# Kernel tuning notes

Measured on AMD Instinct MI355X. Metric: run time of the kernel, lower is better.

## Reference

```python
import jax, jax.numpy as jnp
import numpy as np
import math

B, I, O, D, H = 32, 1152, 10, 16, 10
SUB = 0.8
S = math.ceil(SUB * I)  # 922 subset size


def _safe_l2norm(x, axis, keepdims=False):
    # L2 norm with zero-safe gradient (forward-identical to jnp.linalg.norm)
    s = jnp.sum(x * x, axis=axis, keepdims=keepdims)
    return jnp.where(s == 0, 0.0, jnp.sqrt(jnp.where(s == 0, 1.0, s)))


def setup_inputs() -> dict:
    key = jax.random.key(0)
    k1, k2 = jax.random.split(key)
    u_predict = jax.random.normal(k1, (B, I, O, D), dtype=jnp.float32)
    # emulate torch.rand(...).topk(S, dim=1).indices: top-S distinct indices along input_caps
    noise = jax.random.uniform(k2, (B, I, O, H))
    sample_idx = jnp.argsort(-noise, axis=1)[:, :S].astype(jnp.int64)  # [B,S,O,H]
    return {"u_predict": u_predict, "sample_idx": sample_idx}


def reference(u_predict, sample_idx):
    b, i, o, d = u_predict.shape
    h = sample_idx.shape[-1]
    # scatter 0/1 hypothesis mask r: [B,I,O,H]
    bi = jnp.arange(b)[:, None, None, None]
    oi = jnp.arange(o)[None, None, :, None]
    hi = jnp.arange(h)[None, None, None, :]
    r = jnp.zeros((b, i, o, h), u_predict.dtype).at[bi, sample_idx, oi, hi].set(1.0)

    # Vr = V_exp * r; since r is 0/1, ||Vr||_D = r * ||V||_D
    Vnorm = _safe_l2norm(u_predict, axis=3)            # [B,I,O]
    Vr_norm = Vnorm[..., None] * r                     # [B,I,O,H]
    # Mu = sum_i(Vr_norm * Vr) / sum_i Vr_norm  (Vr_norm*Vr = r*||V||*V since r^2=r)
    num = jnp.einsum('bioh,biod->bodh', Vr_norm, u_predict)   # [B,O,D,H]
    Mu = num / jnp.sum(Vr_norm, axis=1)[:, :, None, :]        # [B,O,D,H]

    # losses = sum_i ||V_exp - Mu||_D  -> [B,O,H]
    diff = u_predict[..., None] - Mu[:, None]          # [B,I,O,D,H]
    losses = jnp.sum(_safe_l2norm(diff, axis=3), axis=1)
    min_idx = jnp.argmin(losses, axis=2)               # [B,O]

    # pick best hypothesis's mask per (batch, output_caps)
    final_r = jnp.take_along_axis(r, min_idx[:, None, :, None], axis=3)  # [B,I,O,1]

    # capsule weighted average
    u = u_predict * final_r
    un = _safe_l2norm(u, axis=3, keepdims=True)        # [B,I,O,1]
    v = jnp.sum(u * un, axis=1) / jnp.sum(un, axis=1)  # [B,O,D]
    return v
```

## Files before the change

kernel.cpp:

```cpp
#include <hip/hip_runtime.h>
#include <math.h>


#define B_    32
#define I_    1152
#define O_    10
#define D_    16
#define H_    10
#define S_    922
#define MASKW 36
#define NT    384
#define NW    6
#define RPT   3
#define HH    11

template <int CTRL, int ROWM>
static __device__ __forceinline__ float dpp_f(float v) {
    return __int_as_float(__builtin_amdgcn_update_dpp(
        0, __float_as_int(v), CTRL, ROWM, 0xf, true));
}
static __device__ __forceinline__ float wave_sum_f32(float v) {
    v += dpp_f<0x111, 0xf>(v);
    v += dpp_f<0x112, 0xf>(v);
    v += dpp_f<0x114, 0xf>(v);
    v += dpp_f<0x118, 0xf>(v);
    v += dpp_f<0x142, 0xa>(v);
    v += dpp_f<0x143, 0xc>(v);
    return v;
}
template <int CTRL, int ROWM>
static __device__ __forceinline__ double dpp_d(double v) {
    long long x = __double_as_longlong(v);
    int lo = (int)(unsigned)(x & 0xffffffffLL);
    int hi = (int)(x >> 32);
    lo = __builtin_amdgcn_update_dpp(0, lo, CTRL, ROWM, 0xf, true);
    hi = __builtin_amdgcn_update_dpp(0, hi, CTRL, ROWM, 0xf, true);
    return __longlong_as_double((long long)(unsigned)lo | ((long long)hi << 32));
}
static __device__ __forceinline__ double wave_sum_f64(double v) {
    v += dpp_d<0x111, 0xf>(v);
    v += dpp_d<0x112, 0xf>(v);
    v += dpp_d<0x114, 0xf>(v);
    v += dpp_d<0x118, 0xf>(v);
    v += dpp_d<0x142, 0xa>(v);
    v += dpp_d<0x143, 0xc>(v);
    return v;
}

__global__ __launch_bounds__(NT, 3) void ransac_kernel(
    const float* __restrict__ up,
    const int*   __restrict__ sidx,
    float*       __restrict__ out)
{
    __shared__ unsigned                 mask[H_][MASKW];
    __shared__ __align__(16) float      hred[HH][NW][20];
    __shared__ float                    Mu_s[H_][D_];
    __shared__ double                   lpart[H_][NW];
    __shared__ double                   losses[H_];
    __shared__ int                      hstar;

    const int blk = blockIdx.x;
    const int xcd = blk & 7, g = blk >> 3;
    const int b   = xcd + 8 * (g / O_);
    const int o   = g - O_ * (g / O_);
    const int bo  = b * O_ + o;

    const int tid  = threadIdx.x;
    const int lane = tid & 63;
    const int wv   = tid >> 6;

    if (tid < H_ * MASKW) ((unsigned*)mask)[tid] = 0u;
    __syncthreads();

    const int* sb = sidx + (size_t)b * (S_ * O_ * H_) + o * H_;
    const bool p2 = tid < (S_ - 2 * NT);
    const int2* ps0 = (const int2*)(sb + (size_t)tid * (O_ * H_));
    const int2* ps1 = (const int2*)(sb + (size_t)(tid + NT) * (O_ * H_));
    int2 a0 = ps0[0], a1 = ps0[1], a2 = ps0[2], a3 = ps0[3], a4 = ps0[4];
    int2 b0 = ps1[0], b1 = ps1[1], b2 = ps1[2], b3 = ps1[3], b4 = ps1[4];
    int2 c0 = {0,0}, c1 = {0,0}, c2 = {0,0}, c3 = {0,0}, c4 = {0,0};
    if (p2) {
        const int2* ps2 = (const int2*)(sb + (size_t)(tid + 2 * NT) * (O_ * H_));
        c0 = ps2[0]; c1 = ps2[1]; c2 = ps2[2]; c3 = ps2[3]; c4 = ps2[4];
    }

    const float* ub = up + ((size_t)b * I_ * O_ + o) * D_;
    float4 R[RPT][4];
    #pragma unroll
    for (int r = 0; r < RPT; ++r) {
        const float4* p = (const float4*)(ub + (size_t)(tid + r * NT) * (O_ * D_));
        R[r][0] = p[0]; R[r][1] = p[1]; R[r][2] = p[2]; R[r][3] = p[3];
    }

    {
        int v0[H_] = {a0.x, a0.y, a1.x, a1.y, a2.x, a2.y, a3.x, a3.y, a4.x, a4.y};
        #pragma unroll
        for (int h = 0; h < H_; ++h)
            atomicOr(&mask[h][v0[h] >> 5], 1u << (v0[h] & 31));
        int v1[H_] = {b0.x, b0.y, b1.x, b1.y, b2.x, b2.y, b3.x, b3.y, b4.x, b4.y};
        #pragma unroll
        for (int h = 0; h < H_; ++h)
            atomicOr(&mask[h][v1[h] >> 5], 1u << (v1[h] & 31));
        if (p2) {
            int v2[H_] = {c0.x, c0.y, c1.x, c1.y, c2.x, c2.y, c3.x, c3.y, c4.x, c4.y};
            #pragma unroll
            for (int h = 0; h < H_; ++h)
                atomicOr(&mask[h][v2[h] >> 5], 1u << (v2[h] & 31));
        }
    }

    float vn[RPT], usq[RPT];
    #pragma unroll
    for (int r = 0; r < RPT; ++r) {
        float4 q0 = R[r][0], q1 = R[r][1], q2 = R[r][2], q3 = R[r][3];
        float s = q0.x*q0.x + q0.y*q0.y + q0.z*q0.z + q0.w*q0.w
                + q1.x*q1.x + q1.y*q1.y + q1.z*q1.z + q1.w*q1.w
                + q2.x*q2.x + q2.y*q2.y + q2.z*q2.z + q2.w*q2.w
                + q3.x*q3.x + q3.y*q3.y + q3.z*q3.z + q3.w*q3.w;
        vn[r] = sqrtf(s);
        float uq[D_] = {q0.x,q0.y,q0.z,q0.w, q1.x,q1.y,q1.z,q1.w,
                        q2.x,q2.y,q2.z,q2.w, q3.x,q3.y,q3.z,q3.w};
        float t = 0.f;
        #pragma unroll
        for (int d = 0; d < D_; ++d) t = fmaf(uq[d], uq[d], t);
        usq[r] = t;
    }
    __syncthreads();

    const int      w0   = tid >> 5;
    const unsigned bitm = 1u << (tid & 31);
    for (int h = 0; h < HH; ++h) {
        float na[17];
        #pragma unroll
        for (int d = 0; d < 17; ++d) na[d] = 0.f;
        #pragma unroll
        for (int r = 0; r < RPT; ++r) {
            float w = vn[r];
            if (h < H_) {
                unsigned mw = mask[h][w0 + 12 * r];
                w = (mw & bitm) ? 0.f : w;
            }
            float4 q0 = R[r][0], q1 = R[r][1], q2 = R[r][2], q3 = R[r][3];
            na[ 0] = fmaf(w, q0.x, na[ 0]); na[ 1] = fmaf(w, q0.y, na[ 1]);
            na[ 2] = fmaf(w, q0.z, na[ 2]); na[ 3] = fmaf(w, q0.w, na[ 3]);
            na[ 4] = fmaf(w, q1.x, na[ 4]); na[ 5] = fmaf(w, q1.y, na[ 5]);
            na[ 6] = fmaf(w, q1.z, na[ 6]); na[ 7] = fmaf(w, q1.w, na[ 7]);
            na[ 8] = fmaf(w, q2.x, na[ 8]); na[ 9] = fmaf(w, q2.y, na[ 9]);
            na[10] = fmaf(w, q2.z, na[10]); na[11] = fmaf(w, q2.w, na[11]);
            na[12] = fmaf(w, q3.x, na[12]); na[13] = fmaf(w, q3.y, na[13]);
            na[14] = fmaf(w, q3.z, na[14]); na[15] = fmaf(w, q3.w, na[15]);
            na[16] += w;
        }
        #pragma unroll
        for (int d = 0; d < 17; ++d) na[d] = wave_sum_f32(na[d]);
        if (lane == 63) {
            *(float4*)&hred[h][wv][ 0] = make_float4(na[ 0], na[ 1], na[ 2], na[ 3]);
            *(float4*)&hred[h][wv][ 4] = make_float4(na[ 4], na[ 5], na[ 6], na[ 7]);
            *(float4*)&hred[h][wv][ 8] = make_float4(na[ 8], na[ 9], na[10], na[11]);
            *(float4*)&hred[h][wv][12] = make_float4(na[12], na[13], na[14], na[15]);
            hred[h][wv][16] = na[16];
        }
    }
    __syncthreads();

    for (int h = wv; h < H_; h += NW) {
        if (lane < D_) {
            float naj = 0.f, totj = 0.f, na16 = 0.f, tot16 = 0.f;
            #pragma unroll
            for (int w = 0; w < NW; ++w) {
                naj   += hred[h ][w][lane];
                totj  += hred[10][w][lane];
                na16  += hred[h ][w][16];
                tot16 += hred[10][w][16];
            }
            float rd = 1.f / (tot16 - na16);
            Mu_s[h][lane] = (totj - naj) * rd;
        }
    }
    __syncthreads();

    for (int h = 0; h < H_; ++h) {
        float4 m0 = *(const float4*)&Mu_s[h][0];
        float4 m1 = *(const float4*)&Mu_s[h][4];
        float4 m2 = *(const float4*)&Mu_s[h][8];
        float4 m3 = *(const float4*)&Mu_s[h][12];
        float mv[D_] = {m0.x, m0.y, m0.z, m0.w, m1.x, m1.y, m1.z, m1.w,
                        m2.x, m2.y, m2.z, m2.w, m3.x, m3.y, m3.z, m3.w};
        float musq = 0.f;
        #pragma unroll
        for (int d = 0; d < D_; ++d) musq = fmaf(mv[d], mv[d], musq);
        double l = 0.0;
        #pragma unroll
        for (int r = 0; r < RPT; ++r) {
            float uq[D_] = {R[r][0].x, R[r][0].y, R[r][0].z, R[r][0].w,
                            R[r][1].x, R[r][1].y, R[r][1].z, R[r][1].w,
                            R[r][2].x, R[r][2].y, R[r][2].z, R[r][2].w,
                            R[r][3].x, R[r][3].y, R[r][3].z, R[r][3].w};
            float dot = 0.f;
            #pragma unroll
            for (int d = 0; d < D_; ++d) dot = fmaf(uq[d], mv[d], dot);
            float d2 = fmaf(-2.f, dot, usq[r] + musq);
            l += (double)sqrtf(fmaxf(d2, 0.f));
        }
        l = wave_sum_f64(l);
        if (lane == 63) lpart[h][wv] = l;
    }
    __syncthreads();

    if (tid < H_) {
        double t = 0.0;
        #pragma unroll
        for (int w = 0; w < NW; ++w) t += lpart[tid][w];
        losses[tid] = t;
    }
    __syncthreads();
    if (tid == 0) {
        int best = 0; double bl = losses[0];
        #pragma unroll
        for (int h = 1; h < H_; ++h)
            if (losses[h] < bl) { bl = losses[h]; best = h; }
        hstar = best;
    }
    __syncthreads();
    if (tid < D_)
        out[(size_t)bo * D_ + tid] = Mu_s[hstar][tid];
}

extern "C" void kernel_launch(void* const* d_in, const int* in_sizes, int n_in,
                              void* d_out, int out_size, void* d_ws, size_t ws_size,
                              hipStream_t stream) {
    const float* up   = (const float*)d_in[0];
    const int*   sidx = (const int*)d_in[1];
    float*       out  = (float*)d_out;
    ransac_kernel<<<B_ * O_, NT, 0, stream>>>(up, sidx, out);
}
```

Before: 104.4 us.

## Split each (b,o) problem across two blocks with global-memory spin handshakes

Each (batch, output-capsule) problem now runs on two 192-thread blocks, each owning half of the input capsules, instead of one 384-thread block. Partial hypothesis sums and partial losses are exchanged through workspace memory, with atomic counters and spin-waits used as inter-block barriers. A memset clears the flags on every launch. The aim is more concurrent blocks across CUs and a shorter per-block critical path, at the cost of global round-trips, spin-waiting, an extra memset launch, and a deadlock risk if the two blocks of a pair are not co-resident.

```diff
diff --git a/kernel.cpp b/kernel.cpp
--- a/kernel.cpp
+++ b/kernel.cpp
@@ -8,11 +8,15 @@
 #define D_    16
 #define H_    10
 #define S_    922
-#define MASKW 36
-#define NT    384
-#define NW    6
+#define NT    192
+#define NW    3
 #define RPT   3
+#define HROWS 576
 #define HH    11
+#define NPAIR 320
+
+#define WS_LOSS_OFF  0x80000u
+#define WS_FLAG_OFF  0x100000u
 
 template <int CTRL, int ROWM>
 static __device__ __forceinline__ float dpp_f(float v) {
@@ -47,65 +51,73 @@
     return v;
 }
 
-__global__ __launch_bounds__(NT, 3) void ransac_kernel(
-    const float* __restrict__ up,
-    const int*   __restrict__ sidx,
-    float*       __restrict__ out)
+__global__ __launch_bounds__(NT, 3) void ransac_half(
+    const float*  __restrict__ up,
+    const int*    __restrict__ sidx,
+    float*        __restrict__ out,
+    float*        __restrict__ hredG,
+    double*       __restrict__ lossG,
+    int*          __restrict__ flag1,
+    int*          __restrict__ flag2)
 {
-    __shared__ unsigned                 mask[H_][MASKW];
-    __shared__ __align__(16) float      hred[HH][NW][20];
-    __shared__ float                    Mu_s[H_][D_];
-    __shared__ double                   lpart[H_][NW];
-    __shared__ double                   losses[H_];
-    __shared__ int                      hstar;
-
-    const int blk = blockIdx.x;
-    const int xcd = blk & 7, g = blk >> 3;
-    const int b   = xcd + 8 * (g / O_);
-    const int o   = g - O_ * (g / O_);
+    __shared__ unsigned mask[H_][HROWS / 32];
+    __shared__ float    hredl[HH][NW][17];
+    __shared__ float    comb[HH][17];
+    __shared__ float    Mu_s[H_][D_];
+    __shared__ double   lpart[H_][NW];
+    __shared__ double   lossc[H_];
+    __shared__ int      hstar;
+
+    const int blk  = blockIdx.x;
+    const int p    = blk >> 1;
+    const int half = blk & 1;
+    const int xcd = p & 7, g = p >> 3;
+    const int gg  = g / O_;
+    const int b   = xcd + 8 * gg;
+    const int o   = g - O_ * gg;
     const int bo  = b * O_ + o;
+    const int r0  = half * HROWS;
 
     const int tid  = threadIdx.x;
     const int lane = tid & 63;
     const int wv   = tid >> 6;
 
-    if (tid < H_ * MASKW) ((unsigned*)mask)[tid] = 0u;
+    if (tid < H_ * (HROWS / 32)) ((unsigned*)mask)[tid] = 0u;
     __syncthreads();
 
     const int* sb = sidx + (size_t)b * (S_ * O_ * H_) + o * H_;
-    const bool p2 = tid < (S_ - 2 * NT);
-    const int2* ps0 = (const int2*)(sb + (size_t)tid * (O_ * H_));
-    const int2* ps1 = (const int2*)(sb + (size_t)(tid + NT) * (O_ * H_));
-    int2 a0 = ps0[0], a1 = ps0[1], a2 = ps0[2], a3 = ps0[3], a4 = ps0[4];
-    int2 b0 = ps1[0], b1 = ps1[1], b2 = ps1[2], b3 = ps1[3], b4 = ps1[4];
-    int2 c0 = {0,0}, c1 = {0,0}, c2 = {0,0}, c3 = {0,0}, c4 = {0,0};
-    if (p2) {
-        const int2* ps2 = (const int2*)(sb + (size_t)(tid + 2 * NT) * (O_ * H_));
-        c0 = ps2[0]; c1 = ps2[1]; c2 = ps2[2]; c3 = ps2[3]; c4 = ps2[4];
+    int2 sv[5][5];
+    #pragma unroll
+    for (int seg = 0; seg < 5; ++seg) {
+        int s = tid + seg * NT;
+        if (s < S_) {
+            const int2* ps = (const int2*)(sb + (size_t)s * (O_ * H_));
+            sv[seg][0]=ps[0]; sv[seg][1]=ps[1]; sv[seg][2]=ps[2];
+            sv[seg][3]=ps[3]; sv[seg][4]=ps[4];
+        } else {
+            int2 m1 = make_int2(-1, -1);
+            sv[seg][0]=m1; sv[seg][1]=m1; sv[seg][2]=m1;
+            sv[seg][3]=m1; sv[seg][4]=m1;
+        }
     }
 
     const float* ub = up + ((size_t)b * I_ * O_ + o) * D_;
     float4 R[RPT][4];
     #pragma unroll
     for (int r = 0; r < RPT; ++r) {
-        const float4* p = (const float4*)(ub + (size_t)(tid + r * NT) * (O_ * D_));
-        R[r][0] = p[0]; R[r][1] = p[1]; R[r][2] = p[2]; R[r][3] = p[3];
-    }
-
-    {
-        int v0[H_] = {a0.x, a0.y, a1.x, a1.y, a2.x, a2.y, a3.x, a3.y, a4.x, a4.y};
-        #pragma unroll
-        for (int h = 0; h < H_; ++h)
-            atomicOr(&mask[h][v0[h] >> 5], 1u << (v0[h] & 31));
-        int v1[H_] = {b0.x, b0.y, b1.x, b1.y, b2.x, b2.y, b3.x, b3.y, b4.x, b4.y};
-        #pragma unroll
-        for (int h = 0; h < H_; ++h)
-            atomicOr(&mask[h][v1[h] >> 5], 1u << (v1[h] & 31));
-        if (p2) {
-            int v2[H_] = {c0.x, c0.y, c1.x, c1.y, c2.x, c2.y, c3.x, c3.y, c4.x, c4.y};
-            #pragma unroll
-            for (int h = 0; h < H_; ++h)
-                atomicOr(&mask[h][v2[h] >> 5], 1u << (v2[h] & 31));
+        const float4* pr = (const float4*)(ub + (size_t)(r0 + tid + r * NT) * (O_ * D_));
+        R[r][0]=pr[0]; R[r][1]=pr[1]; R[r][2]=pr[2]; R[r][3]=pr[3];
+    }
+
+    #pragma unroll
+    for (int seg = 0; seg < 5; ++seg) {
+        int v[H_] = {sv[seg][0].x, sv[seg][0].y, sv[seg][1].x, sv[seg][1].y,
+                     sv[seg][2].x, sv[seg][2].y, sv[seg][3].x, sv[seg][3].y,
+                     sv[seg][4].x, sv[seg][4].y};
+        #pragma unroll
+        for (int h = 0; h < H_; ++h) {
+            unsigned j = (unsigned)(v[h] - r0);
+            if (j < HROWS) atomicOr(&mask[h][j >> 5], 1u << (j & 31));
         }
     }
 
@@ -137,7 +149,7 @@
         for (int r = 0; r < RPT; ++r) {
             float w = vn[r];
             if (h < H_) {
-                unsigned mw = mask[h][w0 + 12 * r];
+                unsigned mw = mask[h][w0 + 6 * r];
                 w = (mw & bitm) ? 0.f : w;
             }
             float4 q0 = R[r][0], q1 = R[r][1], q2 = R[r][2], q3 = R[r][3];
@@ -154,28 +166,36 @@
         #pragma unroll
         for (int d = 0; d < 17; ++d) na[d] = wave_sum_f32(na[d]);
         if (lane == 63) {
-            *(float4*)&hred[h][wv][ 0] = make_float4(na[ 0], na[ 1], na[ 2], na[ 3]);
-            *(float4*)&hred[h][wv][ 4] = make_float4(na[ 4], na[ 5], na[ 6], na[ 7]);
-            *(float4*)&hred[h][wv][ 8] = make_float4(na[ 8], na[ 9], na[10], na[11]);
-            *(float4*)&hred[h][wv][12] = make_float4(na[12], na[13], na[14], na[15]);
-            hred[h][wv][16] = na[16];
-        }
-    }
-    __syncthreads();
-
-    for (int h = wv; h < H_; h += NW) {
-        if (lane < D_) {
-            float naj = 0.f, totj = 0.f, na16 = 0.f, tot16 = 0.f;
             #pragma unroll
-            for (int w = 0; w < NW; ++w) {
-                naj   += hred[h ][w][lane];
-                totj  += hred[10][w][lane];
-                na16  += hred[h ][w][16];
-                tot16 += hred[10][w][16];
-            }
-            float rd = 1.f / (tot16 - na16);
-            Mu_s[h][lane] = (totj - naj) * rd;
-        }
+            for (int d = 0; d < 17; ++d) hredl[h][wv][d] = na[d];
+        }
+    }
+    __syncthreads();
+
+    if (tid < HH * 17) {
+        int h = tid / 17, d = tid - 17 * h;
+        float v = hredl[h][0][d] + hredl[h][1][d] + hredl[h][2][d];
+        hredG[(((size_t)p * 2 + half) * HH + h) * 17 + d] = v;
+    }
+    __threadfence();
+    __syncthreads();
+    if (tid == 0) {
+        atomicAdd(&flag1[p], 1);
+        while (atomicAdd(&flag1[p], 0) < 2) __builtin_amdgcn_s_sleep(2);
+    }
+    __syncthreads();
+    __threadfence();
+
+    if (tid < HH * 17) {
+        int h = tid / 17, d = tid - 17 * h;
+        comb[h][d] = hredG[(((size_t)p * 2 + 0) * HH + h) * 17 + d]
+                   + hredG[(((size_t)p * 2 + 1) * HH + h) * 17 + d];
+    }
+    __syncthreads();
+    if (tid < H_ * D_) {
+        int h = tid >> 4, d = tid & 15;
+        float rd = 1.f / (comb[10][16] - comb[h][16]);
+        Mu_s[h][d] = (comb[10][d] - comb[h][d]) * rd;
     }
     __syncthreads();
 
@@ -208,17 +228,28 @@
     __syncthreads();
 
     if (tid < H_) {
-        double t = 0.0;
-        #pragma unroll
-        for (int w = 0; w < NW; ++w) t += lpart[tid][w];
-        losses[tid] = t;
-    }
-    __syncthreads();
+        double t = lpart[tid][0] + lpart[tid][1] + lpart[tid][2];
+        lossG[((size_t)p * 2 + half) * H_ + tid] = t;
+    }
+    __threadfence();
+    __syncthreads();
+    if (tid == 0) atomicAdd(&flag2[p], 1);
+    if (half) return;
+
     if (tid == 0) {
-        int best = 0; double bl = losses[0];
+        while (atomicAdd(&flag2[p], 0) < 2) __builtin_amdgcn_s_sleep(2);
+    }
+    __syncthreads();
+    __threadfence();
+    if (tid < H_)
+        lossc[tid] = lossG[((size_t)p * 2 + 0) * H_ + tid]
+                   + lossG[((size_t)p * 2 + 1) * H_ + tid];
+    __syncthreads();
+    if (tid == 0) {
+        int best = 0; double bl = lossc[0];
         #pragma unroll
         for (int h = 1; h < H_; ++h)
-            if (losses[h] < bl) { bl = losses[h]; best = h; }
+            if (lossc[h] < bl) { bl = lossc[h]; best = h; }
         hstar = best;
     }
     __syncthreads();
@@ -232,5 +263,11 @@
     const float* up   = (const float*)d_in[0];
     const int*   sidx = (const int*)d_in[1];
     float*       out  = (float*)d_out;
-    ransac_kernel<<<B_ * O_, NT, 0, stream>>>(up, sidx, out);
-}
+    float*  hredG = (float*)d_ws;
+    double* lossG = (double*)((char*)d_ws + WS_LOSS_OFF);
+    int*    flag1 = (int*)((char*)d_ws + WS_FLAG_OFF);
+    int*    flag2 = flag1 + 512;
+    hipMemsetAsync((char*)d_ws + WS_FLAG_OFF, 0, 4096, stream);
+    ransac_half<<<2 * NPAIR, NT, 0, stream>>>(up, sidx, out,
+                                              hredG, lossG, flag1, flag2);
+}
```

Result: slower. 203.8 us (+95.3%).

## Split mask construction into a separate coalesced pre-pass kernel

Applied to the files above, without the earlier changes.

Adds a first kernel that reads sample_idx in contiguous int4 chunks per batch slice and builds partial bitmasks in shared memory, then writes 8 partial mask sets to workspace. The main kernel then ORs the partial masks instead of doing strided int2 gathers and shared atomics itself. The aim is to replace the poorly coalesced index reads in the main kernel with coalesced streaming reads. The cost is an extra kernel launch, a workspace round trip, and per-element modulo/divide arithmetic in the pre-pass.

```diff
diff --git a/kernel.cpp b/kernel.cpp
--- a/kernel.cpp
+++ b/kernel.cpp
@@ -13,6 +13,10 @@
 #define NW    6
 #define RPT   3
 #define HH    11
+#define NSLOT 8
+#define SCH   116
+#define K0NT  256
+#define MWORDS (O_ * H_ * MASKW)
 
 template <int CTRL, int ROWM>
 static __device__ __forceinline__ float dpp_f(float v) {
@@ -47,10 +51,47 @@
     return v;
 }
 
-__global__ __launch_bounds__(NT, 3) void ransac_kernel(
-    const float* __restrict__ up,
-    const int*   __restrict__ sidx,
-    float*       __restrict__ out)
+__global__ __launch_bounds__(K0NT, 2) void ransac_masks(
+    const int*  __restrict__ sidx,
+    unsigned*   __restrict__ maskG)
+{
+    __shared__ unsigned lm[MWORDS];
+    const int blk = blockIdx.x;
+    const int b = blk & 31, k = blk >> 5;
+    const int tid = threadIdx.x;
+
+    for (int t = tid; t < MWORDS; t += K0NT) lm[t] = 0u;
+    __syncthreads();
+
+    const int s0  = k * SCH;
+    const int cnt = min(S_ - s0, SCH);
+    const int n4  = cnt * 25;
+    const int4* base = (const int4*)(sidx + (size_t)b * (S_ * O_ * H_)
+                                          + (size_t)s0 * (O_ * H_));
+    for (int j4 = tid; j4 < n4; j4 += K0NT) {
+        int4 v = base[j4];
+        int vv[4] = {v.x, v.y, v.z, v.w};
+        int j = j4 * 4;
+        #pragma unroll
+        for (int e = 0; e < 4; ++e) {
+            int jj  = j + e;
+            int rem = jj % 100;
+            int o   = rem / 10;
+            int h   = rem - 10 * o;
+            int val = vv[e];
+            atomicOr(&lm[(o * H_ + h) * MASKW + (val >> 5)], 1u << (val & 31));
+        }
+    }
+    __syncthreads();
+
+    unsigned* dst = maskG + (size_t)blk * MWORDS;
+    for (int t = tid; t < MWORDS; t += K0NT) dst[t] = lm[t];
+}
+
+__global__ __launch_bounds__(NT, 3) void ransac_main(
+    const float*    __restrict__ up,
+    const unsigned* __restrict__ maskG,
+    float*          __restrict__ out)
 {
     __shared__ unsigned                 mask[H_][MASKW];
     __shared__ __align__(16) float      hred[HH][NW][20];
@@ -61,27 +102,21 @@
 
     const int blk = blockIdx.x;
     const int xcd = blk & 7, g = blk >> 3;
-    const int b   = xcd + 8 * (g / O_);
-    const int o   = g - O_ * (g / O_);
+    const int gg  = g / O_;
+    const int b   = xcd + 8 * gg;
+    const int o   = g - O_ * gg;
     const int bo  = b * O_ + o;
 
     const int tid  = threadIdx.x;
     const int lane = tid & 63;
     const int wv   = tid >> 6;
 
-    if (tid < H_ * MASKW) ((unsigned*)mask)[tid] = 0u;
-    __syncthreads();
-
-    const int* sb = sidx + (size_t)b * (S_ * O_ * H_) + o * H_;
-    const bool p2 = tid < (S_ - 2 * NT);
-    const int2* ps0 = (const int2*)(sb + (size_t)tid * (O_ * H_));
-    const int2* ps1 = (const int2*)(sb + (size_t)(tid + NT) * (O_ * H_));
-    int2 a0 = ps0[0], a1 = ps0[1], a2 = ps0[2], a3 = ps0[3], a4 = ps0[4];
-    int2 b0 = ps1[0], b1 = ps1[1], b2 = ps1[2], b3 = ps1[3], b4 = ps1[4];
-    int2 c0 = {0,0}, c1 = {0,0}, c2 = {0,0}, c3 = {0,0}, c4 = {0,0};
-    if (p2) {
-        const int2* ps2 = (const int2*)(sb + (size_t)(tid + 2 * NT) * (O_ * H_));
-        c0 = ps2[0]; c1 = ps2[1]; c2 = ps2[2]; c3 = ps2[3]; c4 = ps2[4];
+    unsigned mw8[NSLOT];
+    const bool mt = tid < H_ * MASKW;
+    if (mt) {
+        #pragma unroll
+        for (int k = 0; k < NSLOT; ++k)
+            mw8[k] = maskG[(size_t)(k * 32 + b) * MWORDS + o * (H_ * MASKW) + tid];
     }
 
     const float* ub = up + ((size_t)b * I_ * O_ + o) * D_;
@@ -92,21 +127,11 @@
         R[r][0] = p[0]; R[r][1] = p[1]; R[r][2] = p[2]; R[r][3] = p[3];
     }
 
-    {
-        int v0[H_] = {a0.x, a0.y, a1.x, a1.y, a2.x, a2.y, a3.x, a3.y, a4.x, a4.y};
-        #pragma unroll
-        for (int h = 0; h < H_; ++h)
-            atomicOr(&mask[h][v0[h] >> 5], 1u << (v0[h] & 31));
-        int v1[H_] = {b0.x, b0.y, b1.x, b1.y, b2.x, b2.y, b3.x, b3.y, b4.x, b4.y};
-        #pragma unroll
-        for (int h = 0; h < H_; ++h)
-            atomicOr(&mask[h][v1[h] >> 5], 1u << (v1[h] & 31));
-        if (p2) {
-            int v2[H_] = {c0.x, c0.y, c1.x, c1.y, c2.x, c2.y, c3.x, c3.y, c4.x, c4.y};
-            #pragma unroll
-            for (int h = 0; h < H_; ++h)
-                atomicOr(&mask[h][v2[h] >> 5], 1u << (v2[h] & 31));
-        }
+    if (mt) {
+        unsigned m = mw8[0];
+        #pragma unroll
+        for (int k = 1; k < NSLOT; ++k) m |= mw8[k];
+        ((unsigned*)mask)[tid] = m;
     }
 
     float vn[RPT], usq[RPT];
@@ -232,5 +257,7 @@
     const float* up   = (const float*)d_in[0];
     const int*   sidx = (const int*)d_in[1];
     float*       out  = (float*)d_out;
-    ransac_kernel<<<B_ * O_, NT, 0, stream>>>(up, sidx, out);
-}
+    unsigned*    maskG = (unsigned*)d_ws;
+    ransac_masks<<<NSLOT * B_, K0NT, 0, stream>>>(sidx, maskG);
+    ransac_main<<<B_ * O_, NT, 0, stream>>>(up, maskG, out);
+}
```

After: 110.5 us. +5.9%, slower.

## Process each (b,o) task with a single wave using register-resident rows

Applied to the files above, without the earlier changes.

Shrinks each block from 384 threads to one 64-lane wave that holds 18 contiguous rows per lane in registers. All cross-wave shared-memory reductions and most barriers are replaced by DPP wave sums plus readlane broadcasts, and the argmin is tracked in registers. The goal is to remove synchronisation and LDS traffic. In exchange each block gets far fewer threads: only 320 single-wave blocks run on the device, register pressure from 72 float4s per lane is high, and each lane loads strided rows, which risks lower latency hiding and worse coalescing.

```diff
diff --git a/kernel.cpp b/kernel.cpp
--- a/kernel.cpp
+++ b/kernel.cpp
@@ -8,11 +8,8 @@
 #define D_    16
 #define H_    10
 #define S_    922
-#define MASKW 36
-#define NT    384
-#define NW    6
-#define RPT   3
-#define HH    11
+#define MASKW 37
+#define RPT   18
 
 template <int CTRL, int ROWM>
 static __device__ __forceinline__ float dpp_f(float v) {
@@ -47,69 +44,57 @@
     return v;
 }
 
-__global__ __launch_bounds__(NT, 3) void ransac_kernel(
+static __device__ __forceinline__ float bcast63_f(float v) {
+    return __int_as_float(__builtin_amdgcn_readlane(__float_as_int(v), 63));
+}
+static __device__ __forceinline__ double bcast63_d(double v) {
+    long long x = __double_as_longlong(v);
+    int lo = __builtin_amdgcn_readlane((int)(unsigned)(x & 0xffffffffLL), 63);
+    int hi = __builtin_amdgcn_readlane((int)(x >> 32), 63);
+    return __longlong_as_double((long long)(unsigned)lo | ((long long)hi << 32));
+}
+
+static __device__ __forceinline__ void task_bo(int p, int& b, int& o) {
+    int xcd = p & 7, g = p >> 3;
+    int gg = g / O_;
+    b = xcd + 8 * gg;
+    o = g - O_ * gg;
+}
+
+__global__ __launch_bounds__(64, 1) void ransac_kernel(
     const float* __restrict__ up,
     const int*   __restrict__ sidx,
     float*       __restrict__ out)
 {
-    __shared__ unsigned                 mask[H_][MASKW];
-    __shared__ __align__(16) float      hred[HH][NW][20];
-    __shared__ float                    Mu_s[H_][D_];
-    __shared__ double                   lpart[H_][NW];
-    __shared__ double                   losses[H_];
-    __shared__ int                      hstar;
+    __shared__ unsigned mask[H_][MASKW];
 
     const int blk = blockIdx.x;
-    const int xcd = blk & 7, g = blk >> 3;
-    const int b   = xcd + 8 * (g / O_);
-    const int o   = g - O_ * (g / O_);
+    int b, o; task_bo(blk, b, o);
     const int bo  = b * O_ + o;
-
-    const int tid  = threadIdx.x;
-    const int lane = tid & 63;
-    const int wv   = tid >> 6;
-
-    if (tid < H_ * MASKW) ((unsigned*)mask)[tid] = 0u;
+    const int tid = threadIdx.x;
+
+    for (int t = tid; t < H_ * MASKW; t += 64) ((unsigned*)mask)[t] = 0u;
     __syncthreads();
 
     const int* sb = sidx + (size_t)b * (S_ * O_ * H_) + o * H_;
-    const bool p2 = tid < (S_ - 2 * NT);
-    const int2* ps0 = (const int2*)(sb + (size_t)tid * (O_ * H_));
-    const int2* ps1 = (const int2*)(sb + (size_t)(tid + NT) * (O_ * H_));
-    int2 a0 = ps0[0], a1 = ps0[1], a2 = ps0[2], a3 = ps0[3], a4 = ps0[4];
-    int2 b0 = ps1[0], b1 = ps1[1], b2 = ps1[2], b3 = ps1[3], b4 = ps1[4];
-    int2 c0 = {0,0}, c1 = {0,0}, c2 = {0,0}, c3 = {0,0}, c4 = {0,0};
-    if (p2) {
-        const int2* ps2 = (const int2*)(sb + (size_t)(tid + 2 * NT) * (O_ * H_));
-        c0 = ps2[0]; c1 = ps2[1]; c2 = ps2[2]; c3 = ps2[3]; c4 = ps2[4];
+    for (int s = tid; s < S_; s += 64) {
+        const int2* ps = (const int2*)(sb + (size_t)s * (O_ * H_));
+        int2 a0 = ps[0], a1 = ps[1], a2 = ps[2], a3 = ps[3], a4 = ps[4];
+        int v[H_] = {a0.x, a0.y, a1.x, a1.y, a2.x, a2.y, a3.x, a3.y, a4.x, a4.y};
+        #pragma unroll
+        for (int h = 0; h < H_; ++h)
+            atomicOr(&mask[h][v[h] >> 5], 1u << (v[h] & 31));
     }
 
     const float* ub = up + ((size_t)b * I_ * O_ + o) * D_;
     float4 R[RPT][4];
     #pragma unroll
     for (int r = 0; r < RPT; ++r) {
-        const float4* p = (const float4*)(ub + (size_t)(tid + r * NT) * (O_ * D_));
+        const float4* p = (const float4*)(ub + (size_t)(tid * RPT + r) * (O_ * D_));
         R[r][0] = p[0]; R[r][1] = p[1]; R[r][2] = p[2]; R[r][3] = p[3];
     }
 
-    {
-        int v0[H_] = {a0.x, a0.y, a1.x, a1.y, a2.x, a2.y, a3.x, a3.y, a4.x, a4.y};
-        #pragma unroll
-        for (int h = 0; h < H_; ++h)
-            atomicOr(&mask[h][v0[h] >> 5], 1u << (v0[h] & 31));
-        int v1[H_] = {b0.x, b0.y, b1.x, b1.y, b2.x, b2.y, b3.x, b3.y, b4.x, b4.y};
-        #pragma unroll
-        for (int h = 0; h < H_; ++h)
-            atomicOr(&mask[h][v1[h] >> 5], 1u << (v1[h] & 31));
-        if (p2) {
-            int v2[H_] = {c0.x, c0.y, c1.x, c1.y, c2.x, c2.y, c3.x, c3.y, c4.x, c4.y};
-            #pragma unroll
-            for (int h = 0; h < H_; ++h)
-                atomicOr(&mask[h][v2[h] >> 5], 1u << (v2[h] & 31));
-        }
-    }
-
-    float vn[RPT], usq[RPT];
+    float vn[RPT];
     #pragma unroll
     for (int r = 0; r < RPT; ++r) {
         float4 q0 = R[r][0], q1 = R[r][1], q2 = R[r][2], q3 = R[r][3];
@@ -118,28 +103,17 @@
                 + q2.x*q2.x + q2.y*q2.y + q2.z*q2.z + q2.w*q2.w
                 + q3.x*q3.x + q3.y*q3.y + q3.z*q3.z + q3.w*q3.w;
         vn[r] = sqrtf(s);
-        float uq[D_] = {q0.x,q0.y,q0.z,q0.w, q1.x,q1.y,q1.z,q1.w,
-                        q2.x,q2.y,q2.z,q2.w, q3.x,q3.y,q3.z,q3.w};
-        float t = 0.f;
-        #pragma unroll
-        for (int d = 0; d < D_; ++d) t = fmaf(uq[d], uq[d], t);
-        usq[r] = t;
     }
     __syncthreads();
 
-    const int      w0   = tid >> 5;
-    const unsigned bitm = 1u << (tid & 31);
-    for (int h = 0; h < HH; ++h) {
+    float tot[17];
+    {
         float na[17];
         #pragma unroll
         for (int d = 0; d < 17; ++d) na[d] = 0.f;
         #pragma unroll
         for (int r = 0; r < RPT; ++r) {
             float w = vn[r];
-            if (h < H_) {
-                unsigned mw = mask[h][w0 + 12 * r];
-                w = (mw & bitm) ? 0.f : w;
-            }
             float4 q0 = R[r][0], q1 = R[r][1], q2 = R[r][2], q3 = R[r][3];
             na[ 0] = fmaf(w, q0.x, na[ 0]); na[ 1] = fmaf(w, q0.y, na[ 1]);
             na[ 2] = fmaf(w, q0.z, na[ 2]); na[ 3] = fmaf(w, q0.w, na[ 3]);
@@ -152,78 +126,89 @@
             na[16] += w;
         }
         #pragma unroll
-        for (int d = 0; d < 17; ++d) na[d] = wave_sum_f32(na[d]);
-        if (lane == 63) {
-            *(float4*)&hred[h][wv][ 0] = make_float4(na[ 0], na[ 1], na[ 2], na[ 3]);
-            *(float4*)&hred[h][wv][ 4] = make_float4(na[ 4], na[ 5], na[ 6], na[ 7]);
-            *(float4*)&hred[h][wv][ 8] = make_float4(na[ 8], na[ 9], na[10], na[11]);
-            *(float4*)&hred[h][wv][12] = make_float4(na[12], na[13], na[14], na[15]);
-            hred[h][wv][16] = na[16];
+        for (int d = 0; d < 17; ++d) tot[d] = bcast63_f(wave_sum_f32(na[d]));
+    }
+
+    float usq[RPT];
+    #pragma unroll
+    for (int r = 0; r < RPT; ++r) {
+        float4 q0 = R[r][0], q1 = R[r][1], q2 = R[r][2], q3 = R[r][3];
+        float uq[D_] = {q0.x,q0.y,q0.z,q0.w, q1.x,q1.y,q1.z,q1.w,
+                        q2.x,q2.y,q2.z,q2.w, q3.x,q3.y,q3.z,q3.w};
+        float t = 0.f;
+        #pragma unroll
+        for (int d = 0; d < D_; ++d) t = fmaf(uq[d], uq[d], t);
+        usq[r] = t;
+    }
+
+    const int bit0 = tid * RPT;
+    double bl = 0.0;
+    float  mb[D_];
+    #pragma unroll
+    for (int d = 0; d < D_; ++d) mb[d] = 0.f;
+
+    for (int h = 0; h < H_; ++h) {
+        unsigned lo = mask[h][bit0 >> 5];
+        unsigned hi = mask[h][(bit0 >> 5) + 1];
+        unsigned mbits = (unsigned)(((((unsigned long long)hi) << 32) | lo)
+                                    >> (bit0 & 31));
+
+        float na[17];
+        #pragma unroll
+        for (int d = 0; d < 17; ++d) na[d] = 0.f;
+        #pragma unroll
+        for (int r = 0; r < RPT; ++r) {
+            float w = (mbits & (1u << r)) ? 0.f : vn[r];
+            float4 q0 = R[r][0], q1 = R[r][1], q2 = R[r][2], q3 = R[r][3];
+            na[ 0] = fmaf(w, q0.x, na[ 0]); na[ 1] = fmaf(w, q0.y, na[ 1]);
+            na[ 2] = fmaf(w, q0.z, na[ 2]); na[ 3] = fmaf(w, q0.w, na[ 3]);
+            na[ 4] = fmaf(w, q1.x, na[ 4]); na[ 5] = fmaf(w, q1.y, na[ 5]);
+            na[ 6] = fmaf(w, q1.z, na[ 6]); na[ 7] = fmaf(w, q1.w, na[ 7]);
+            na[ 8] = fmaf(w, q2.x, na[ 8]); na[ 9] = fmaf(w, q2.y, na[ 9]);
+            na[10] = fmaf(w, q2.z, na[10]); na[11] = fmaf(w, q2.w, na[11]);
+            na[12] = fmaf(w, q3.x, na[12]); na[13] = fmaf(w, q3.y, na[13]);
+            na[14] = fmaf(w, q3.z, na[14]); na[15] = fmaf(w, q3.w, na[15]);
+            na[16] += w;
         }
-    }
-    __syncthreads();
-
-    for (int h = wv; h < H_; h += NW) {
-        if (lane < D_) {
-            float naj = 0.f, totj = 0.f, na16 = 0.f, tot16 = 0.f;
-            #pragma unroll
-            for (int w = 0; w < NW; ++w) {
-                naj   += hred[h ][w][lane];
-                totj  += hred[10][w][lane];
-                na16  += hred[h ][w][16];
-                tot16 += hred[10][w][16];
-            }
-            float rd = 1.f / (tot16 - na16);
-            Mu_s[h][lane] = (totj - naj) * rd;
-        }
-    }
-    __syncthreads();
-
-    for (int h = 0; h < H_; ++h) {
-        float4 m0 = *(const float4*)&Mu_s[h][0];
-        float4 m1 = *(const float4*)&Mu_s[h][4];
-        float4 m2 = *(const float4*)&Mu_s[h][8];
-        float4 m3 = *(const float4*)&Mu_s[h][12];
-        float mv[D_] = {m0.x, m0.y, m0.z, m0.w, m1.x, m1.y, m1.z, m1.w,
-                        m2.x, m2.y, m2.z, m2.w, m3.x, m3.y, m3.z, m3.w};
+        float sa[17];
+        #pragma unroll
+        for (int d = 0; d < 17; ++d) sa[d] = bcast63_f(wave_sum_f32(na[d]));
+
+        float rd = 1.f / (tot[16] - sa[16]);
+        float mv[D_];
+        #pragma unroll
+        for (int d = 0; d < D_; ++d) mv[d] = (tot[d] - sa[d]) * rd;
         float musq = 0.f;
         #pragma unroll
         for (int d = 0; d < D_; ++d) musq = fmaf(mv[d], mv[d], musq);
+
         double l = 0.0;
         #pragma unroll
         for (int r = 0; r < RPT; ++r) {
-            float uq[D_] = {R[r][0].x, R[r][0].y, R[r][0].z, R[r][0].w,
-                            R[r][1].x, R[r][1].y, R[r][1].z, R[r][1].w,
-                            R[r][2].x, R[r][2].y, R[r][2].z, R[r][2].w,
-                            R[r][3].x, R[r][3].y, R[r][3].z, R[r][3].w};
+            float4 q0 = R[r][0], q1 = R[r][1], q2 = R[r][2], q3 = R[r][3];
+            float uq[D_] = {q0.x,q0.y,q0.z,q0.w, q1.x,q1.y,q1.z,q1.w,
+                            q2.x,q2.y,q2.z,q2.w, q3.x,q3.y,q3.z,q3.w};
             float dot = 0.f;
             #pragma unroll
             for (int d = 0; d < D_; ++d) dot = fmaf(uq[d], mv[d], dot);
             float d2 = fmaf(-2.f, dot, usq[r] + musq);
             l += (double)sqrtf(fmaxf(d2, 0.f));
         }
-        l = wave_sum_f64(l);
-        if (lane == 63) lpart[h][wv] = l;
-    }
-    __syncthreads();
-
-    if (tid < H_) {
-        double t = 0.0;
-        #pragma unroll
-        for (int w = 0; w < NW; ++w) t += lpart[tid][w];
-        losses[tid] = t;
-    }
-    __syncthreads();
+        double ls = bcast63_d(wave_sum_f64(l));
+
+        bool better = (h == 0) || (ls < bl);
+        bl = better ? ls : bl;
+        #pragma unroll
+        for (int d = 0; d < D_; ++d) mb[d] = better ? mv[d] : mb[d];
+    }
+
     if (tid == 0) {
-        int best = 0; double bl = losses[0];
-        #pragma unroll
-        for (int h = 1; h < H_; ++h)
-            if (losses[h] < bl) { bl = losses[h]; best = h; }
-        hstar = best;
-    }
-    __syncthreads();
-    if (tid < D_)
-        out[(size_t)bo * D_ + tid] = Mu_s[hstar][tid];
+        float* op = out + (size_t)bo * D_;
+        *(float4*)(op +  0) = make_float4(mb[ 0], mb[ 1], mb[ 2], mb[ 3]);
+        *(float4*)(op +  4) = make_float4(mb[ 4], mb[ 5], mb[ 6], mb[ 7]);
+        *(float4*)(op +  8) = make_float4(mb[ 8], mb[ 9], mb[10], mb[11]);
+        *(float4*)(op + 12) = make_float4(mb[12], mb[13], mb[14], mb[15]);
+    }
 }
 
 extern "C" void kernel_launch(void* const* d_in, const int* in_sizes, int n_in,
@@ -232,5 +217,5 @@
     const float* up   = (const float*)d_in[0];
     const int*   sidx = (const int*)d_in[1];
     float*       out  = (float*)d_out;
-    ransac_kernel<<<B_ * O_, NT, 0, stream>>>(up, sidx, out);
-}
+    ransac_kernel<<<B_ * O_, 64, 0, stream>>>(up, sidx, out);
+}
```

Measured after the change: 161.8 us. +55.1%, slower.
